# Performance work log

Hardware: AMD Instinct MI355X
Metric: run time of the kernel (lower is better)

## Reference

```python
import jax, jax.numpy as jnp
import numpy as np

N_MBED = 384
HEAD_SIZE = 64

def setup_inputs() -> dict:
    key = jax.random.key(0)
    kx, kq, kk, kv = jax.random.split(key, 4)
    B, T = 128, 256
    x = jax.random.normal(kx, (B, T, N_MBED), dtype=jnp.float32)
    # torch nn.Linear(n_mbed, head_size, bias=False): y = x @ W^T, W:[head_size, n_mbed].
    # We store the transposed weight [n_mbed, head_size] so y = x @ W.
    s = 1.0 / np.sqrt(N_MBED)
    Wq = jax.random.uniform(kq, (N_MBED, HEAD_SIZE), jnp.float32, -s, s)
    Wk = jax.random.uniform(kk, (N_MBED, HEAD_SIZE), jnp.float32, -s, s)
    Wv = jax.random.uniform(kv, (N_MBED, HEAD_SIZE), jnp.float32, -s, s)
    return {"x": x, "Wq": Wq, "Wk": Wk, "Wv": Wv}

def reference(x, Wq, Wk, Wv):
    B, T, C = x.shape  # C = n_mbed = 384
    q = x @ Wq  # [B,T,H]
    k = x @ Wk
    v = x @ Wv
    # Faithful to source: wei = k @ q^T, scaled by C**-0.5 (C = n_mbed, not head_size)
    wei = jnp.einsum('bth,bsh->bts', k, q) * (C ** -0.5)  # [B,T,T]
    mask = jnp.tril(jnp.ones((T, T), dtype=bool))
    wei = jnp.where(mask, wei, -jnp.inf)
    wei = jax.nn.softmax(wei, axis=-1)
    # dropout omitted (eval mode / identity)
    out = jnp.einsum('bts,bsh->bth', wei, v)  # [B,T,H]
    return out
```

## Files before the change

kernel.cpp:

```cpp
#include <hip/hip_runtime.h>
#include <hip/hip_bf16.h>
#include <math.h>

constexpr int kB = 128;
constexpr int kT = 256;
constexpr int kC = 384;
constexpr int kH = 64;

using bf16x8 = __attribute__((ext_vector_type(8))) short;
using f32x4  = __attribute__((ext_vector_type(4))) float;

union BF4 { short4 s; __hip_bfloat162 h[2]; };

__device__ inline short4 cvt4(float4 a) {
    BF4 u;
    u.h[0] = __float22bfloat162_rn(float2{a.x, a.y});
    u.h[1] = __float22bfloat162_rn(float2{a.z, a.w});
    return u.s;
}
__device__ inline short bf1(float f) {
    __hip_bfloat16 h = __float2bfloat16(f);
    return *(short*)&h;
}

__global__ void prep_kernel(const float* __restrict__ Wq,
                            const float* __restrict__ Wk,
                            const float* __restrict__ Wv,
                            __hip_bfloat16* __restrict__ Wt) {
    int idx = blockIdx.x * 256 + threadIdx.x;
    int n = idx / kC, c = idx % kC;
    int w = n >> 6, h = n & 63;
    const float* W = (w == 0) ? Wq : (w == 1) ? Wk : Wv;
    float val = W[c * kH + h];
    if (w == 1) val *= 0.051031036307982884f;
    Wt[idx] = __float2bfloat16(val);
}

__global__ __launch_bounds__(512, 2) void fused_kernel(
    const float* __restrict__ x, const __hip_bfloat16* __restrict__ Wt,
    float* __restrict__ out)
{
    __shared__ short Qs[256 * 72];
    __shared__ short Ks[128 * 72];
    __shared__ short VTs[64 * 264];
    __shared__ short As[2][256 * 36];
    __shared__ short Bs[2][192 * 36];

    const int bid  = blockIdx.x;
    const int b    = ((bid >> 4) << 3) | (bid & 7);
    const int half = ((bid >> 3) & 1) ^ 1;
    const int t0   = half * 128;

    const int tid  = threadIdx.x;
    const int wave = tid >> 6, lane = tid & 63;
    const int m16  = lane & 15, quad = lane >> 4;
    const int wm = wave & 1, wn = wave >> 1;
    const short* wt = (const short*)Wt;
    const float* xb = x + (size_t)b * kT * kC;

    const bool mfmaAct = (half == 1) || (wm == 0);

    bool kskip[3];
#pragma unroll
    for (int j = 0; j < 3; ++j) {
        const int nt = wn * 3 + j;
        kskip[j] = (half == 1) && (wm == 0) && (nt >= 4) && (nt < 8);
    }

    const int arow = tid >> 1, acol = (tid & 1) * 16;
    const bool aAct = (half == 1) || (arow < 128);

    float4 la0[4], la1[4]; bf16x8 lb0a, lb0b, lb1a, lb1b;
    auto glod = [&](float4* la, bf16x8& lba, bf16x8& lbb, int k0) {
        if (aAct) {
#pragma unroll
            for (int i = 0; i < 4; ++i)
                la[i] = *(const float4*)(xb + (size_t)arow * kC + k0 + acol + 4 * i);
        }
        {
            int n = tid >> 2, kk = (tid & 3) * 8;
            lba = *(const bf16x8*)(wt + (size_t)n * kC + k0 + kk);
        }
        if (tid < 256) {
            int c = tid + 512;
            int n = c >> 2, kk = (c & 3) * 8;
            lbb = *(const bf16x8*)(wt + (size_t)n * kC + k0 + kk);
        }
    };
    auto swr = [&](int d, const float4* la, const bf16x8& lba, const bf16x8& lbb) {
        if (aAct) {
#pragma unroll
            for (int i = 0; i < 4; ++i)
                *(short4*)&As[d][arow * 36 + acol + 4 * i] = cvt4(la[i]);
        }
        {
            int n = tid >> 2, kk = (tid & 3) * 8;
            *(bf16x8*)&Bs[d][n * 36 + kk] = lba;
        }
        if (tid < 256) {
            int c = tid + 512;
            int n = c >> 2, kk = (c & 3) * 8;
            *(bf16x8*)&Bs[d][n * 36 + kk] = lbb;
        }
    };

    f32x4 acc[8][3];
#pragma unroll
    for (int mt = 0; mt < 8; ++mt)
#pragma unroll
        for (int j = 0; j < 3; ++j) acc[mt][j] = f32x4{0.f, 0.f, 0.f, 0.f};

    auto mstep = [&](int d) {
        if (!mfmaAct) return;
        bf16x8 af[8];
#pragma unroll
        for (int mt = 0; mt < 8; ++mt)
            af[mt] = *(const bf16x8*)&As[d][(wm * 128 + mt * 16 + m16) * 36 + quad * 8];
#pragma unroll
        for (int j = 0; j < 3; ++j) {
            if (!kskip[j]) {
                const bf16x8 bfr =
                    *(const bf16x8*)&Bs[d][((wn * 3 + j) * 16 + m16) * 36 + quad * 8];
#pragma unroll
                for (int mt = 0; mt < 8; ++mt)
                    acc[mt][j] = __builtin_amdgcn_mfma_f32_16x16x32_bf16(
                        af[mt], bfr, acc[mt][j], 0, 0, 0);
            }
        }
    };

    glod(la0, lb0a, lb0b, 0);
    glod(la1, lb1a, lb1b, 32);
    swr(0, la0, lb0a, lb0b);
    __syncthreads();

    for (int s = 0; s < 12; s += 2) {
        if (s < 10) glod(la0, lb0a, lb0b, (s + 2) * 32);
        mstep(0);
        swr(1, la1, lb1a, lb1b);
        __syncthreads();
        if (s + 1 < 10) glod(la1, lb1a, lb1b, (s + 3) * 32);
        mstep(1);
        if (s + 1 < 11) swr(0, la0, lb0a, lb0b);
        __syncthreads();
    }

    if (mfmaAct) {
#pragma unroll
        for (int mt = 0; mt < 8; ++mt) {
            const int mbase = wm * 128 + mt * 16 + quad * 4;
#pragma unroll
            for (int j = 0; j < 3; ++j) {
                const int nt = wn * 3 + j;
                const int w  = nt >> 2;
                const int h  = (nt & 3) * 16 + m16;
                if (w == 2) {
                    float4 f = make_float4(acc[mt][j][0], acc[mt][j][1],
                                           acc[mt][j][2], acc[mt][j][3]);
                    *(short4*)&VTs[h * 264 + mbase] = cvt4(f);
                } else if (w == 1) {
                    if ((mbase >> 7) == half) {
#pragma unroll
                        for (int r = 0; r < 4; ++r)
                            Ks[(mbase + r - t0) * 72 + h] = bf1(acc[mt][j][r]);
                    }
                } else {
#pragma unroll
                    for (int r = 0; r < 4; ++r)
                        Qs[(mbase + r) * 72 + h] = bf1(acc[mt][j][r]);
                }
            }
        }
    }
    __syncthreads();

    const int wband = t0 + wave * 16;
    short* Pb = &As[0][0] + wave * 1152;

    const bf16x8 ka0 = *(const bf16x8*)&Ks[(wave * 16 + m16) * 72 + quad * 8];
    const bf16x8 ka1 = *(const bf16x8*)&Ks[(wave * 16 + m16) * 72 + quad * 8 + 32];

    const int ilast = wband >> 6;
    const int jmaxd = wave & 3;

    f32x4 S[4][4];
    const f32x4 Z = f32x4{0.f, 0.f, 0.f, 0.f};
#pragma unroll
    for (int i = 0; i < 4; ++i)
#pragma unroll
        for (int j = 0; j < 4; ++j) S[i][j] = Z;

    __builtin_amdgcn_s_setprio(1);
#pragma unroll
    for (int i = 0; i < 4; ++i) {
        if (i <= ilast) {
#pragma unroll
            for (int j = 0; j < 4; ++j) {
                if (i < ilast || j <= jmaxd) {
                    const int s = i * 64 + j * 16 + m16;
                    bf16x8 qb0 = *(const bf16x8*)&Qs[s * 72 + quad * 8];
                    bf16x8 qb1 = *(const bf16x8*)&Qs[s * 72 + quad * 8 + 32];
                    S[i][j] = __builtin_amdgcn_mfma_f32_16x16x32_bf16(qb0, ka0, S[i][j], 0, 0, 0);
                    S[i][j] = __builtin_amdgcn_mfma_f32_16x16x32_bf16(qb1, ka1, S[i][j], 0, 0, 0);
                }
            }
        }
    }
    __builtin_amdgcn_s_setprio(0);

#pragma unroll
    for (int i = 0; i < 4; ++i)
#pragma unroll
        for (int j = 0; j < 4; ++j)
            if (i == ilast && j == jmaxd) {
#pragma unroll
                for (int r = 0; r < 4; ++r)
                    if (quad * 4 + r > m16) S[i][j][r] = -INFINITY;
            }

    float rm = -INFINITY;
#pragma unroll
    for (int i = 0; i < 4; ++i)
#pragma unroll
        for (int j = 0; j < 4; ++j)
            if (i <= ilast && (i < ilast || j <= jmaxd))
#pragma unroll
                for (int r = 0; r < 4; ++r) rm = fmaxf(rm, S[i][j][r]);
    rm = fmaxf(rm, __shfl_xor(rm, 16, 64));
    rm = fmaxf(rm, __shfl_xor(rm, 32, 64));

    float l_ = 0.f;
#pragma unroll
    for (int i = 0; i < 4; ++i)
#pragma unroll
        for (int j = 0; j < 4; ++j)
            if (i <= ilast && (i < ilast || j <= jmaxd))
#pragma unroll
                for (int r = 0; r < 4; ++r) {
                    const float e = __expf(S[i][j][r] - rm);
                    S[i][j][r] = e;
                    l_ += e;
                }
    l_ += __shfl_xor(l_, 16, 64);
    l_ += __shfl_xor(l_, 32, 64);

    f32x4 O[4];
#pragma unroll
    for (int i = 0; i < 4; ++i) O[i] = f32x4{0.f, 0.f, 0.f, 0.f};

#pragma unroll
    for (int i = 0; i < 4; ++i) {
        if (i <= ilast) {
#pragma unroll
            for (int j = 0; j < 4; ++j)
#pragma unroll
                for (int p = 0; p < 2; ++p) {
                    __hip_bfloat162 w = __float22bfloat162_rn(
                        float2{S[i][j][2 * p], S[i][j][2 * p + 1]});
                    *(__hip_bfloat162*)&Pb[m16 * 72 + j * 16 + quad * 4 + 2 * p] = w;
                }
            bf16x8 pf0 = *(const bf16x8*)&Pb[m16 * 72 + quad * 8];
            bf16x8 pf1 = *(const bf16x8*)&Pb[m16 * 72 + quad * 8 + 32];

            __builtin_amdgcn_s_setprio(1);
#pragma unroll
            for (int ht = 0; ht < 4; ++ht) {
                bf16x8 vb0 = *(const bf16x8*)&VTs[(ht * 16 + m16) * 264 + i * 64 + quad * 8];
                bf16x8 vb1 = *(const bf16x8*)&VTs[(ht * 16 + m16) * 264 + i * 64 + quad * 8 + 32];
                O[ht] = __builtin_amdgcn_mfma_f32_16x16x32_bf16(pf0, vb0, O[ht], 0, 0, 0);
                O[ht] = __builtin_amdgcn_mfma_f32_16x16x32_bf16(pf1, vb1, O[ht], 0, 0, 0);
            }
            __builtin_amdgcn_s_setprio(0);
        }
    }

    float lbc[4];
#pragma unroll
    for (int r = 0; r < 4; ++r)
        lbc[r] = __shfl(l_, (quad << 4) | (quad * 4 + r), 64);
#pragma unroll
    for (int r = 0; r < 4; ++r) {
        const float inv = 1.f / lbc[r];
        const size_t row = (size_t)(b * kT + wband + quad * 4 + r);
#pragma unroll
        for (int ht = 0; ht < 4; ++ht)
            out[row * kH + ht * 16 + m16] = O[ht][r] * inv;
    }
}

extern "C" void kernel_launch(void* const* d_in, const int* in_sizes, int n_in,
                              void* d_out, int out_size, void* d_ws, size_t ws_size,
                              hipStream_t stream) {
    const float* x  = (const float*)d_in[0];
    const float* Wq = (const float*)d_in[1];
    const float* Wk = (const float*)d_in[2];
    const float* Wv = (const float*)d_in[3];
    float* out = (float*)d_out;

    __hip_bfloat16* Wt = (__hip_bfloat16*)d_ws;

    prep_kernel<<<(192 * kC) / 256, 256, 0, stream>>>(Wq, Wk, Wv, Wt);
    fused_kernel<<<dim3(256), 512, 0, stream>>>(x, Wt, out);
}
```

Before: 110.7 us.

## Alias shared buffers, swizzle Q/K/V layouts, shuffle P in registers, raise occupancy

Overlays the projection staging buffers and the Q/K/VT attention buffers in a single 80KB shared array instead of separate allocations, and raises launch bounds to request 4 blocks per CU. Q/K and V^T switch from padded rows to XOR-swizzled unpadded layouts to avoid bank conflicts, the P matrix is rearranged via cross-lane shuffles instead of an LDS round-trip, and the projection loop drops its second register prefetch set. The aim is higher occupancy and less LDS traffic. The cost is more shuffles and tighter register budgets that may spill.

```diff
diff --git a/kernel.cpp b/kernel.cpp
--- a/kernel.cpp
+++ b/kernel.cpp
@@ -36,15 +36,18 @@
     Wt[idx] = __float2bfloat16(val);
 }
 
-__global__ __launch_bounds__(512, 2) void fused_kernel(
+__global__ __launch_bounds__(512, 4) void fused_kernel(
     const float* __restrict__ x, const __hip_bfloat16* __restrict__ Wt,
     float* __restrict__ out)
 {
-    __shared__ short Qs[256 * 72];
-    __shared__ short Ks[128 * 72];
-    __shared__ short VTs[64 * 264];
-    __shared__ short As[2][256 * 36];
-    __shared__ short Bs[2][192 * 36];
+    __shared__ __align__(16) short SM[40960];
+    short* Qs  = SM;
+    short* Ks  = SM + 16384;
+    short* VTs = SM + 24576;
+    short* As0 = SM;
+    short* As1 = SM + 9216;
+    short* Bs0 = SM + 18432;
+    short* Bs1 = SM + 25344;
 
     const int bid  = blockIdx.x;
     const int b    = ((bid >> 4) << 3) | (bid & 7);
@@ -58,6 +61,9 @@
     const short* wt = (const short*)Wt;
     const float* xb = x + (size_t)b * kT * kC;
 
+    auto QI = [](int s, int h) { return ((s << 6) + h) ^ ((s & 7) << 3); };
+    auto VI = [](int h, int s) { return ((h << 8) + s) ^ ((h & 7) << 3); };
+
     const bool mfmaAct = (half == 1) || (wm == 0);
 
     bool kskip[3];
@@ -70,8 +76,8 @@
     const int arow = tid >> 1, acol = (tid & 1) * 16;
     const bool aAct = (half == 1) || (arow < 128);
 
-    float4 la0[4], la1[4]; bf16x8 lb0a, lb0b, lb1a, lb1b;
-    auto glod = [&](float4* la, bf16x8& lba, bf16x8& lbb, int k0) {
+    float4 la[4]; bf16x8 lb0, lb1;
+    auto glod = [&](int k0) {
         if (aAct) {
 #pragma unroll
             for (int i = 0; i < 4; ++i)
@@ -79,28 +85,30 @@
         }
         {
             int n = tid >> 2, kk = (tid & 3) * 8;
-            lba = *(const bf16x8*)(wt + (size_t)n * kC + k0 + kk);
+            lb0 = *(const bf16x8*)(wt + (size_t)n * kC + k0 + kk);
         }
         if (tid < 256) {
             int c = tid + 512;
             int n = c >> 2, kk = (c & 3) * 8;
-            lbb = *(const bf16x8*)(wt + (size_t)n * kC + k0 + kk);
+            lb1 = *(const bf16x8*)(wt + (size_t)n * kC + k0 + kk);
         }
     };
-    auto swr = [&](int d, const float4* la, const bf16x8& lba, const bf16x8& lbb) {
+    auto swr = [&](int d) {
+        short* Ad = d ? As1 : As0;
+        short* Bd = d ? Bs1 : Bs0;
         if (aAct) {
 #pragma unroll
             for (int i = 0; i < 4; ++i)
-                *(short4*)&As[d][arow * 36 + acol + 4 * i] = cvt4(la[i]);
+                *(short4*)&Ad[arow * 36 + acol + 4 * i] = cvt4(la[i]);
         }
         {
             int n = tid >> 2, kk = (tid & 3) * 8;
-            *(bf16x8*)&Bs[d][n * 36 + kk] = lba;
+            *(bf16x8*)&Bd[n * 36 + kk] = lb0;
         }
         if (tid < 256) {
             int c = tid + 512;
             int n = c >> 2, kk = (c & 3) * 8;
-            *(bf16x8*)&Bs[d][n * 36 + kk] = lbb;
+            *(bf16x8*)&Bd[n * 36 + kk] = lb1;
         }
     };
 
@@ -112,15 +120,17 @@
 
     auto mstep = [&](int d) {
         if (!mfmaAct) return;
+        const short* Ad = d ? As1 : As0;
+        const short* Bd = d ? Bs1 : Bs0;
         bf16x8 af[8];
 #pragma unroll
         for (int mt = 0; mt < 8; ++mt)
-            af[mt] = *(const bf16x8*)&As[d][(wm * 128 + mt * 16 + m16) * 36 + quad * 8];
+            af[mt] = *(const bf16x8*)&Ad[(wm * 128 + mt * 16 + m16) * 36 + quad * 8];
 #pragma unroll
         for (int j = 0; j < 3; ++j) {
             if (!kskip[j]) {
                 const bf16x8 bfr =
-                    *(const bf16x8*)&Bs[d][((wn * 3 + j) * 16 + m16) * 36 + quad * 8];
+                    *(const bf16x8*)&Bd[((wn * 3 + j) * 16 + m16) * 36 + quad * 8];
 #pragma unroll
                 for (int mt = 0; mt < 8; ++mt)
                     acc[mt][j] = __builtin_amdgcn_mfma_f32_16x16x32_bf16(
@@ -129,19 +139,15 @@
         }
     };
 
-    glod(la0, lb0a, lb0b, 0);
-    glod(la1, lb1a, lb1b, 32);
-    swr(0, la0, lb0a, lb0b);
+    glod(0);
+    swr(0);
     __syncthreads();
 
-    for (int s = 0; s < 12; s += 2) {
-        if (s < 10) glod(la0, lb0a, lb0b, (s + 2) * 32);
-        mstep(0);
-        swr(1, la1, lb1a, lb1b);
-        __syncthreads();
-        if (s + 1 < 10) glod(la1, lb1a, lb1b, (s + 3) * 32);
-        mstep(1);
-        if (s + 1 < 11) swr(0, la0, lb0a, lb0b);
+    for (int s = 0; s < 12; ++s) {
+        const int d = s & 1;
+        if (s < 11) glod((s + 1) * 32);
+        mstep(d);
+        if (s < 11) swr(d ^ 1);
         __syncthreads();
     }
 
@@ -157,17 +163,17 @@
                 if (w == 2) {
                     float4 f = make_float4(acc[mt][j][0], acc[mt][j][1],
                                            acc[mt][j][2], acc[mt][j][3]);
-                    *(short4*)&VTs[h * 264 + mbase] = cvt4(f);
+                    *(short4*)&VTs[VI(h, mbase)] = cvt4(f);
                 } else if (w == 1) {
                     if ((mbase >> 7) == half) {
 #pragma unroll
                         for (int r = 0; r < 4; ++r)
-                            Ks[(mbase + r - t0) * 72 + h] = bf1(acc[mt][j][r]);
+                            Ks[QI(mbase + r - t0, h)] = bf1(acc[mt][j][r]);
                     }
                 } else {
 #pragma unroll
                     for (int r = 0; r < 4; ++r)
-                        Qs[(mbase + r) * 72 + h] = bf1(acc[mt][j][r]);
+                        Qs[QI(mbase + r, h)] = bf1(acc[mt][j][r]);
                 }
             }
         }
@@ -175,13 +181,11 @@
     __syncthreads();
 
     const int wband = t0 + wave * 16;
-    short* Pb = &As[0][0] + wave * 1152;
-
-    const bf16x8 ka0 = *(const bf16x8*)&Ks[(wave * 16 + m16) * 72 + quad * 8];
-    const bf16x8 ka1 = *(const bf16x8*)&Ks[(wave * 16 + m16) * 72 + quad * 8 + 32];
-
     const int ilast = wband >> 6;
     const int jmaxd = wave & 3;
+
+    const bf16x8 ka0 = *(const bf16x8*)&Ks[QI(wave * 16 + m16, quad * 8)];
+    const bf16x8 ka1 = *(const bf16x8*)&Ks[QI(wave * 16 + m16, quad * 8 + 32)];
 
     f32x4 S[4][4];
     const f32x4 Z = f32x4{0.f, 0.f, 0.f, 0.f};
@@ -198,8 +202,8 @@
             for (int j = 0; j < 4; ++j) {
                 if (i < ilast || j <= jmaxd) {
                     const int s = i * 64 + j * 16 + m16;
-                    bf16x8 qb0 = *(const bf16x8*)&Qs[s * 72 + quad * 8];
-                    bf16x8 qb1 = *(const bf16x8*)&Qs[s * 72 + quad * 8 + 32];
+                    bf16x8 qb0 = *(const bf16x8*)&Qs[QI(s, quad * 8)];
+                    bf16x8 qb1 = *(const bf16x8*)&Qs[QI(s, quad * 8 + 32)];
                     S[i][j] = __builtin_amdgcn_mfma_f32_16x16x32_bf16(qb0, ka0, S[i][j], 0, 0, 0);
                     S[i][j] = __builtin_amdgcn_mfma_f32_16x16x32_bf16(qb1, ka1, S[i][j], 0, 0, 0);
                 }
@@ -248,27 +252,40 @@
 #pragma unroll
     for (int i = 0; i < 4; ++i) O[i] = f32x4{0.f, 0.f, 0.f, 0.f};
 
+    const int l0 = (quad & 1) * 32 + m16;
 #pragma unroll
     for (int i = 0; i < 4; ++i) {
         if (i <= ilast) {
+            unsigned Wp[4][2];
 #pragma unroll
             for (int j = 0; j < 4; ++j)
 #pragma unroll
-                for (int p = 0; p < 2; ++p) {
-                    __hip_bfloat162 w = __float22bfloat162_rn(
-                        float2{S[i][j][2 * p], S[i][j][2 * p + 1]});
-                    *(__hip_bfloat162*)&Pb[m16 * 72 + j * 16 + quad * 4 + 2 * p] = w;
-                }
-            bf16x8 pf0 = *(const bf16x8*)&Pb[m16 * 72 + quad * 8];
-            bf16x8 pf1 = *(const bf16x8*)&Pb[m16 * 72 + quad * 8 + 32];
+                for (int u = 0; u < 2; ++u) {
+                    __hip_bfloat162 t2 = __float22bfloat162_rn(
+                        float2{S[i][j][2 * u], S[i][j][2 * u + 1]});
+                    Wp[j][u] = *(unsigned*)&t2;
+                }
+            unsigned pw0[4], pw1[4];
+#pragma unroll
+            for (int j = 0; j < 4; ++j)
+#pragma unroll
+                for (int u = 0; u < 2; ++u) {
+                    unsigned v0 = (unsigned)__shfl((int)Wp[j][u], l0, 64);
+                    unsigned v1 = (unsigned)__shfl((int)Wp[j][u], l0 + 16, 64);
+                    if ((quad >> 1) == j)     { pw0[u] = v0; pw0[2 + u] = v1; }
+                    if ((quad >> 1) == j - 2) { pw1[u] = v0; pw1[2 + u] = v1; }
+                }
+            union { unsigned u[4]; bf16x8 v; } Pf0, Pf1;
+#pragma unroll
+            for (int w = 0; w < 4; ++w) { Pf0.u[w] = pw0[w]; Pf1.u[w] = pw1[w]; }
 
             __builtin_amdgcn_s_setprio(1);
 #pragma unroll
             for (int ht = 0; ht < 4; ++ht) {
-                bf16x8 vb0 = *(const bf16x8*)&VTs[(ht * 16 + m16) * 264 + i * 64 + quad * 8];
-                bf16x8 vb1 = *(const bf16x8*)&VTs[(ht * 16 + m16) * 264 + i * 64 + quad * 8 + 32];
-                O[ht] = __builtin_amdgcn_mfma_f32_16x16x32_bf16(pf0, vb0, O[ht], 0, 0, 0);
-                O[ht] = __builtin_amdgcn_mfma_f32_16x16x32_bf16(pf1, vb1, O[ht], 0, 0, 0);
+                bf16x8 vb0 = *(const bf16x8*)&VTs[VI(ht * 16 + m16, i * 64 + quad * 8)];
+                bf16x8 vb1 = *(const bf16x8*)&VTs[VI(ht * 16 + m16, i * 64 + quad * 8 + 32)];
+                O[ht] = __builtin_amdgcn_mfma_f32_16x16x32_bf16(Pf0.v, vb0, O[ht], 0, 0, 0);
+                O[ht] = __builtin_amdgcn_mfma_f32_16x16x32_bf16(Pf1.v, vb1, O[ht], 0, 0, 0);
             }
             __builtin_amdgcn_s_setprio(0);
         }
```

After: 223.8 us. +102.1%, slower.

## Load projection operands directly from global memory, drop LDS staging and P scratch

Applied to the files above, without the earlier changes.

The QKV projection no longer stages x and W through double-buffered LDS tiles with block-wide barriers. Each wave now loads its own x rows straight from global memory, converts them to bf16 in registers, and reads weight fragments directly from global or L2 for all 12 output tiles. The P-matrix relayout for the PV MFMA uses cross-lane shuffles instead of an LDS scratch round trip. This frees LDS and removes the syncs of the projection loop, which may allow higher occupancy. In exchange, every wave re-reads the full weight matrix from global memory and global loads are no longer prefetched ahead of the MFMAs.

```diff
diff --git a/kernel.cpp b/kernel.cpp
--- a/kernel.cpp
+++ b/kernel.cpp
@@ -10,8 +10,17 @@
 using bf16x8 = __attribute__((ext_vector_type(8))) short;
 using f32x4  = __attribute__((ext_vector_type(4))) float;
 
+union BF8 { bf16x8 v; __hip_bfloat162 h[4]; };
 union BF4 { short4 s; __hip_bfloat162 h[2]; };
 
+__device__ inline bf16x8 cvt8(float4 a, float4 b) {
+    BF8 u;
+    u.h[0] = __float22bfloat162_rn(float2{a.x, a.y});
+    u.h[1] = __float22bfloat162_rn(float2{a.z, a.w});
+    u.h[2] = __float22bfloat162_rn(float2{b.x, b.y});
+    u.h[3] = __float22bfloat162_rn(float2{b.z, b.w});
+    return u.v;
+}
 __device__ inline short4 cvt4(float4 a) {
     BF4 u;
     u.h[0] = __float22bfloat162_rn(float2{a.x, a.y});
@@ -43,8 +52,6 @@
     __shared__ short Qs[256 * 72];
     __shared__ short Ks[128 * 72];
     __shared__ short VTs[64 * 264];
-    __shared__ short As[2][256 * 36];
-    __shared__ short Bs[2][192 * 36];
 
     const int bid  = blockIdx.x;
     const int b    = ((bid >> 4) << 3) | (bid & 7);
@@ -54,106 +61,57 @@
     const int tid  = threadIdx.x;
     const int wave = tid >> 6, lane = tid & 63;
     const int m16  = lane & 15, quad = lane >> 4;
-    const int wm = wave & 1, wn = wave >> 1;
     const short* wt = (const short*)Wt;
     const float* xb = x + (size_t)b * kT * kC;
 
-    const bool mfmaAct = (half == 1) || (wm == 0);
-
-    bool kskip[3];
-#pragma unroll
-    for (int j = 0; j < 3; ++j) {
-        const int nt = wn * 3 + j;
-        kskip[j] = (half == 1) && (wm == 0) && (nt >= 4) && (nt < 8);
-    }
-
-    const int arow = tid >> 1, acol = (tid & 1) * 16;
-    const bool aAct = (half == 1) || (arow < 128);
-
-    float4 la0[4], la1[4]; bf16x8 lb0a, lb0b, lb1a, lb1b;
-    auto glod = [&](float4* la, bf16x8& lba, bf16x8& lbb, int k0) {
-        if (aAct) {
-#pragma unroll
-            for (int i = 0; i < 4; ++i)
-                la[i] = *(const float4*)(xb + (size_t)arow * kC + k0 + acol + 4 * i);
-        }
+    const int wbase = half ? wave * 32 : wave * 16;
+    const float* xr0 = xb + (size_t)(wbase + m16) * kC;
+    const float* xr1 = xb + (size_t)(wbase + 16 + m16) * kC;
+
+    f32x4 acc[2][12];
+#pragma unroll
+    for (int mt = 0; mt < 2; ++mt)
+#pragma unroll
+        for (int j = 0; j < 12; ++j) acc[mt][j] = f32x4{0.f, 0.f, 0.f, 0.f};
+
+    for (int ks = 0; ks < 12; ++ks) {
+        const int k0 = ks * 32 + quad * 8;
+
+        bf16x8 af0, af1;
         {
-            int n = tid >> 2, kk = (tid & 3) * 8;
-            lba = *(const bf16x8*)(wt + (size_t)n * kC + k0 + kk);
-        }
-        if (tid < 256) {
-            int c = tid + 512;
-            int n = c >> 2, kk = (c & 3) * 8;
-            lbb = *(const bf16x8*)(wt + (size_t)n * kC + k0 + kk);
-        }
-    };
-    auto swr = [&](int d, const float4* la, const bf16x8& lba, const bf16x8& lbb) {
-        if (aAct) {
-#pragma unroll
-            for (int i = 0; i < 4; ++i)
-                *(short4*)&As[d][arow * 36 + acol + 4 * i] = cvt4(la[i]);
-        }
-        {
-            int n = tid >> 2, kk = (tid & 3) * 8;
-            *(bf16x8*)&Bs[d][n * 36 + kk] = lba;
-        }
-        if (tid < 256) {
-            int c = tid + 512;
-            int n = c >> 2, kk = (c & 3) * 8;
-            *(bf16x8*)&Bs[d][n * 36 + kk] = lbb;
-        }
-    };
-
-    f32x4 acc[8][3];
-#pragma unroll
-    for (int mt = 0; mt < 8; ++mt)
-#pragma unroll
-        for (int j = 0; j < 3; ++j) acc[mt][j] = f32x4{0.f, 0.f, 0.f, 0.f};
-
-    auto mstep = [&](int d) {
-        if (!mfmaAct) return;
-        bf16x8 af[8];
-#pragma unroll
-        for (int mt = 0; mt < 8; ++mt)
-            af[mt] = *(const bf16x8*)&As[d][(wm * 128 + mt * 16 + m16) * 36 + quad * 8];
-#pragma unroll
-        for (int j = 0; j < 3; ++j) {
-            if (!kskip[j]) {
+            float4 a = *(const float4*)(xr0 + k0);
+            float4 c = *(const float4*)(xr0 + k0 + 4);
+            af0 = cvt8(a, c);
+        }
+        if (half) {
+            float4 a = *(const float4*)(xr1 + k0);
+            float4 c = *(const float4*)(xr1 + k0 + 4);
+            af1 = cvt8(a, c);
+        }
+
+#pragma unroll
+        for (int j = 0; j < 12; ++j) {
+            const bool skip = half && (wave < 4) && (j >= 4) && (j < 8);
+            if (!skip) {
                 const bf16x8 bfr =
-                    *(const bf16x8*)&Bs[d][((wn * 3 + j) * 16 + m16) * 36 + quad * 8];
-#pragma unroll
-                for (int mt = 0; mt < 8; ++mt)
-                    acc[mt][j] = __builtin_amdgcn_mfma_f32_16x16x32_bf16(
-                        af[mt], bfr, acc[mt][j], 0, 0, 0);
-            }
-        }
-    };
-
-    glod(la0, lb0a, lb0b, 0);
-    glod(la1, lb1a, lb1b, 32);
-    swr(0, la0, lb0a, lb0b);
-    __syncthreads();
-
-    for (int s = 0; s < 12; s += 2) {
-        if (s < 10) glod(la0, lb0a, lb0b, (s + 2) * 32);
-        mstep(0);
-        swr(1, la1, lb1a, lb1b);
-        __syncthreads();
-        if (s + 1 < 10) glod(la1, lb1a, lb1b, (s + 3) * 32);
-        mstep(1);
-        if (s + 1 < 11) swr(0, la0, lb0a, lb0b);
-        __syncthreads();
-    }
-
-    if (mfmaAct) {
-#pragma unroll
-        for (int mt = 0; mt < 8; ++mt) {
-            const int mbase = wm * 128 + mt * 16 + quad * 4;
-#pragma unroll
-            for (int j = 0; j < 3; ++j) {
-                const int nt = wn * 3 + j;
-                const int w  = nt >> 2;
-                const int h  = (nt & 3) * 16 + m16;
+                    *(const bf16x8*)(wt + (size_t)(j * 16 + m16) * kC + k0);
+                acc[0][j] = __builtin_amdgcn_mfma_f32_16x16x32_bf16(
+                    af0, bfr, acc[0][j], 0, 0, 0);
+                if (half)
+                    acc[1][j] = __builtin_amdgcn_mfma_f32_16x16x32_bf16(
+                        af1, bfr, acc[1][j], 0, 0, 0);
+            }
+        }
+    }
+
+#pragma unroll
+    for (int mt = 0; mt < 2; ++mt) {
+        if (mt == 0 || half) {
+            const int mbase = wbase + mt * 16 + quad * 4;
+#pragma unroll
+            for (int j = 0; j < 12; ++j) {
+                const int w = j >> 2;
+                const int h = (j & 3) * 16 + m16;
                 if (w == 2) {
                     float4 f = make_float4(acc[mt][j][0], acc[mt][j][1],
                                            acc[mt][j][2], acc[mt][j][3]);
@@ -175,13 +133,11 @@
     __syncthreads();
 
     const int wband = t0 + wave * 16;
-    short* Pb = &As[0][0] + wave * 1152;
+    const int ilast = wband >> 6;
+    const int jmaxd = wave & 3;
 
     const bf16x8 ka0 = *(const bf16x8*)&Ks[(wave * 16 + m16) * 72 + quad * 8];
     const bf16x8 ka1 = *(const bf16x8*)&Ks[(wave * 16 + m16) * 72 + quad * 8 + 32];
-
-    const int ilast = wband >> 6;
-    const int jmaxd = wave & 3;
 
     f32x4 S[4][4];
     const f32x4 Z = f32x4{0.f, 0.f, 0.f, 0.f};
@@ -248,27 +204,40 @@
 #pragma unroll
     for (int i = 0; i < 4; ++i) O[i] = f32x4{0.f, 0.f, 0.f, 0.f};
 
+    const int l0 = (quad & 1) * 32 + m16;
 #pragma unroll
     for (int i = 0; i < 4; ++i) {
         if (i <= ilast) {
+            unsigned Wp[4][2];
 #pragma unroll
             for (int j = 0; j < 4; ++j)
 #pragma unroll
-                for (int p = 0; p < 2; ++p) {
-                    __hip_bfloat162 w = __float22bfloat162_rn(
-                        float2{S[i][j][2 * p], S[i][j][2 * p + 1]});
-                    *(__hip_bfloat162*)&Pb[m16 * 72 + j * 16 + quad * 4 + 2 * p] = w;
-                }
-            bf16x8 pf0 = *(const bf16x8*)&Pb[m16 * 72 + quad * 8];
-            bf16x8 pf1 = *(const bf16x8*)&Pb[m16 * 72 + quad * 8 + 32];
+                for (int u = 0; u < 2; ++u) {
+                    __hip_bfloat162 t2 = __float22bfloat162_rn(
+                        float2{S[i][j][2 * u], S[i][j][2 * u + 1]});
+                    Wp[j][u] = *(unsigned*)&t2;
+                }
+            unsigned pw0[4], pw1[4];
+#pragma unroll
+            for (int j = 0; j < 4; ++j)
+#pragma unroll
+                for (int u = 0; u < 2; ++u) {
+                    unsigned v0 = (unsigned)__shfl((int)Wp[j][u], l0, 64);
+                    unsigned v1 = (unsigned)__shfl((int)Wp[j][u], l0 + 16, 64);
+                    if ((quad >> 1) == j)     { pw0[u] = v0; pw0[2 + u] = v1; }
+                    if ((quad >> 1) == j - 2) { pw1[u] = v0; pw1[2 + u] = v1; }
+                }
+            union { unsigned u[4]; bf16x8 v; } Pf0, Pf1;
+#pragma unroll
+            for (int w = 0; w < 4; ++w) { Pf0.u[w] = pw0[w]; Pf1.u[w] = pw1[w]; }
 
             __builtin_amdgcn_s_setprio(1);
 #pragma unroll
             for (int ht = 0; ht < 4; ++ht) {
                 bf16x8 vb0 = *(const bf16x8*)&VTs[(ht * 16 + m16) * 264 + i * 64 + quad * 8];
                 bf16x8 vb1 = *(const bf16x8*)&VTs[(ht * 16 + m16) * 264 + i * 64 + quad * 8 + 32];
-                O[ht] = __builtin_amdgcn_mfma_f32_16x16x32_bf16(pf0, vb0, O[ht], 0, 0, 0);
-                O[ht] = __builtin_amdgcn_mfma_f32_16x16x32_bf16(pf1, vb1, O[ht], 0, 0, 0);
+                O[ht] = __builtin_amdgcn_mfma_f32_16x16x32_bf16(Pf0.v, vb0, O[ht], 0, 0, 0);
+                O[ht] = __builtin_amdgcn_mfma_f32_16x16x32_bf16(Pf1.v, vb1, O[ht], 0, 0, 0);
             }
             __builtin_amdgcn_s_setprio(0);
         }
```

After: 133.8 us. +20.9%, slower.

## Use single register prefetch stage in projection loop and fold log2e into K scale

Applied to the files above, without the earlier changes.

The projection GEMM loop drops from two register-staged global prefetches to a single set of prefetch registers, now one step ahead instead of two, with the MFMA step inlined. This lowers register pressure under the 512-thread, 2-block launch bound, at the cost of less global-load latency hiding. Separately, the K weight scale now includes log2(e), so the softmax can use exp2f instead of __expf and skip a multiply per element.

```diff
diff --git a/kernel.cpp b/kernel.cpp
--- a/kernel.cpp
+++ b/kernel.cpp
@@ -32,7 +32,7 @@
     int w = n >> 6, h = n & 63;
     const float* W = (w == 0) ? Wq : (w == 1) ? Wk : Wv;
     float val = W[c * kH + h];
-    if (w == 1) val *= 0.051031036307982884f;
+    if (w == 1) val *= 0.07362222374744683f;
     Wt[idx] = __float2bfloat16(val);
 }
 
@@ -70,8 +70,8 @@
     const int arow = tid >> 1, acol = (tid & 1) * 16;
     const bool aAct = (half == 1) || (arow < 128);
 
-    float4 la0[4], la1[4]; bf16x8 lb0a, lb0b, lb1a, lb1b;
-    auto glod = [&](float4* la, bf16x8& lba, bf16x8& lbb, int k0) {
+    float4 la[4]; bf16x8 lb0, lb1;
+    auto glod = [&](int k0) {
         if (aAct) {
 #pragma unroll
             for (int i = 0; i < 4; ++i)
@@ -79,15 +79,15 @@
         }
         {
             int n = tid >> 2, kk = (tid & 3) * 8;
-            lba = *(const bf16x8*)(wt + (size_t)n * kC + k0 + kk);
+            lb0 = *(const bf16x8*)(wt + (size_t)n * kC + k0 + kk);
         }
         if (tid < 256) {
             int c = tid + 512;
             int n = c >> 2, kk = (c & 3) * 8;
-            lbb = *(const bf16x8*)(wt + (size_t)n * kC + k0 + kk);
+            lb1 = *(const bf16x8*)(wt + (size_t)n * kC + k0 + kk);
         }
     };
-    auto swr = [&](int d, const float4* la, const bf16x8& lba, const bf16x8& lbb) {
+    auto swr = [&](int d) {
         if (aAct) {
 #pragma unroll
             for (int i = 0; i < 4; ++i)
@@ -95,12 +95,12 @@
         }
         {
             int n = tid >> 2, kk = (tid & 3) * 8;
-            *(bf16x8*)&Bs[d][n * 36 + kk] = lba;
+            *(bf16x8*)&Bs[d][n * 36 + kk] = lb0;
         }
         if (tid < 256) {
             int c = tid + 512;
             int n = c >> 2, kk = (c & 3) * 8;
-            *(bf16x8*)&Bs[d][n * 36 + kk] = lbb;
+            *(bf16x8*)&Bs[d][n * 36 + kk] = lb1;
         }
     };
 
@@ -110,38 +110,33 @@
 #pragma unroll
         for (int j = 0; j < 3; ++j) acc[mt][j] = f32x4{0.f, 0.f, 0.f, 0.f};
 
-    auto mstep = [&](int d) {
-        if (!mfmaAct) return;
-        bf16x8 af[8];
-#pragma unroll
-        for (int mt = 0; mt < 8; ++mt)
-            af[mt] = *(const bf16x8*)&As[d][(wm * 128 + mt * 16 + m16) * 36 + quad * 8];
-#pragma unroll
-        for (int j = 0; j < 3; ++j) {
-            if (!kskip[j]) {
-                const bf16x8 bfr =
-                    *(const bf16x8*)&Bs[d][((wn * 3 + j) * 16 + m16) * 36 + quad * 8];
-#pragma unroll
-                for (int mt = 0; mt < 8; ++mt)
-                    acc[mt][j] = __builtin_amdgcn_mfma_f32_16x16x32_bf16(
-                        af[mt], bfr, acc[mt][j], 0, 0, 0);
-            }
-        }
-    };
-
-    glod(la0, lb0a, lb0b, 0);
-    glod(la1, lb1a, lb1b, 32);
-    swr(0, la0, lb0a, lb0b);
+    glod(0);
+    swr(0);
     __syncthreads();
 
-    for (int s = 0; s < 12; s += 2) {
-        if (s < 10) glod(la0, lb0a, lb0b, (s + 2) * 32);
-        mstep(0);
-        swr(1, la1, lb1a, lb1b);
-        __syncthreads();
-        if (s + 1 < 10) glod(la1, lb1a, lb1b, (s + 3) * 32);
-        mstep(1);
-        if (s + 1 < 11) swr(0, la0, lb0a, lb0b);
+    for (int s = 0; s < 12; ++s) {
+        const int d = s & 1;
+        if (s < 11) glod((s + 1) * 32);
+
+        if (mfmaAct) {
+            bf16x8 af[8];
+#pragma unroll
+            for (int mt = 0; mt < 8; ++mt)
+                af[mt] = *(const bf16x8*)&As[d][(wm * 128 + mt * 16 + m16) * 36 + quad * 8];
+#pragma unroll
+            for (int j = 0; j < 3; ++j) {
+                if (!kskip[j]) {
+                    const bf16x8 bfr =
+                        *(const bf16x8*)&Bs[d][((wn * 3 + j) * 16 + m16) * 36 + quad * 8];
+#pragma unroll
+                    for (int mt = 0; mt < 8; ++mt)
+                        acc[mt][j] = __builtin_amdgcn_mfma_f32_16x16x32_bf16(
+                            af[mt], bfr, acc[mt][j], 0, 0, 0);
+                }
+            }
+        }
+
+        if (s < 11) swr(d ^ 1);
         __syncthreads();
     }
 
@@ -237,7 +232,7 @@
             if (i <= ilast && (i < ilast || j <= jmaxd))
 #pragma unroll
                 for (int r = 0; r < 4; ++r) {
-                    const float e = __expf(S[i][j][r] - rm);
+                    const float e = exp2f(S[i][j][r] - rm);
                     S[i][j][r] = e;
                     l_ += e;
                 }
```

Measured after the change: 109.9 us. Within noise of the previous version (-0.7%).
